# Kernel tuning notes

Measured on AMD Instinct MI355X. Metric: run time of the kernel, lower is better.

## Reference

```python
import jax, jax.numpy as jnp
import numpy as np

E, K = 8, 2            # num_experts, top_k
B, T, N, D = 32, 64, 32, 128  # batch, time, n_vars, feature
H = 2                  # heads; head_size = D // 2
EPS = np.finfo(np.float64).eps  # matches np.finfo(float).eps in torch combine


def setup_inputs() -> dict:
    key = jax.random.key(0)
    ks = jax.random.split(key, 7)
    s = 0.02  # small init keeps exp() in combine numerically tame
    x = jax.random.normal(ks[0], (B, T, N, D), dtype=jnp.float32)
    Wg = jax.random.normal(ks[1], (D, E), dtype=jnp.float32) * s
    # per-expert distinct (per-variable) weights: CustomLinear with [N, D, D]
    Wd = jax.random.normal(ks[2], (E, 2, N, D, D), dtype=jnp.float32) * s
    bd = jax.random.normal(ks[3], (E, 2, N, D), dtype=jnp.float32) * s
    # per-expert shared weights: CustomLinear with [D, D], bias [1, D]
    Ws = jax.random.normal(ks[4], (E, 2, D, D), dtype=jnp.float32) * s
    bs = jax.random.normal(ks[5], (E, 2, 1, D), dtype=jnp.float32) * s
    return {"x": x, "Wg": Wg, "Wd": Wd, "bd": bd, "Ws": Ws, "bs": bs}


def _expert(x, Wd, bd, Ws, bs):
    # Intra_Patch_Attention, self-attention over time per variable, 2 heads.
    # Wd: [2,N,D,D], bd: [2,N,D], Ws: [2,D,D], bs: [2,1,D]
    h = D // H
    k = jnp.einsum('btnd,nde->btne', x, Wd[0]) + bd[0]
    v = jnp.einsum('btnd,nde->btne', x, Wd[1]) + bd[1]
    q = x.reshape(B, T, N, H, h)
    k = k.reshape(B, T, N, H, h)
    v = v.reshape(B, T, N, H, h)
    att = jnp.einsum('bqnhd,bknhd->bnhqk', q, k) / np.float32(np.sqrt(h))
    att = jax.nn.softmax(att, axis=-1)
    o = jnp.einsum('bnhqk,bknhd->bqnhd', att, v).reshape(B, T, N, D)
    o = jax.nn.relu(jnp.einsum('btnd,de->btne', o, Ws[0]) + bs[0])
    o = jnp.einsum('btnd,de->btne', o, Ws[1]) + bs[1]
    return o  # [B,T,N,D]


def reference(x, Wg, Wd, bd, Ws, bs):
    # --- noisy-top-k gating (eval mode: no noise) ---
    logits = jnp.mean(x, axis=(1, 2)) @ Wg                  # [B,E]
    top_v, top_i = jax.lax.top_k(logits, K)                 # [B,K]
    top_g = jax.nn.softmax(top_v, axis=-1)
    gates = jnp.zeros((B, E), x.dtype).at[jnp.arange(B)[:, None], top_i].set(top_g)
    # --- per-expert attention (dense == sparse dispatch: gate 0 kills term) ---
    outs = jax.vmap(_expert, in_axes=(None, 0, 0, 0, 0))(x, Wd, bd, Ws, bs)  # [E,B,T,N,D]
    # --- SparseDispatcher.combine: log(index_add(gate * exp(expert_out))) ---
    combined = jnp.einsum('ebtnd,be->btnd', jnp.exp(outs), gates)
    combined = jnp.where(combined == 0, jnp.float32(EPS), combined)
    return jnp.log(combined)
```

## Files before the change

kernel.cpp:

```cpp
#include <hip/hip_runtime.h>

#define B_ 32
#define T_ 64
#define N_ 32
#define D_ 128
#define E_ 8

#define WS_WDT 0u
#define WS_WST 16777216u
#define WS_PART (16777216u + 524288u)
#define WS_NEED (16777216u + 524288u + 262144u)

typedef short          s16x8  __attribute__((ext_vector_type(8)));
typedef float          f32x4  __attribute__((ext_vector_type(4)));
typedef unsigned short u16x8v __attribute__((ext_vector_type(8)));
typedef unsigned short u16x4v __attribute__((ext_vector_type(4)));

#define MFMA(a, b, c) __builtin_amdgcn_mfma_f32_16x16x32_bf16(a, b, c, 0, 0, 0)

__device__ __forceinline__ float b2f(unsigned short u) {
    union { unsigned int i; float f; } v; v.i = ((unsigned int)u) << 16; return v.f;
}
__device__ __forceinline__ unsigned short f2b(float f) {
    union { float f; unsigned int i; } v; v.f = f;
    unsigned int x = v.i;
    unsigned int r = x + 0x7fffu + ((x >> 16) & 1u);
    return (unsigned short)(r >> 16);
}

template <bool BF16>
__device__ __forceinline__ float ld(const void* p, size_t i) {
    if (BF16) return b2f(((const unsigned short*)p)[i]);
    else      return ((const float*)p)[i];
}

__device__ __forceinline__ s16x8 ldBT(const unsigned short* WT, int c, int k0) {
    return *(const s16x8*)(WT + (size_t)c * D_ + k0);
}

__device__ __forceinline__ s16x8 ldA(const unsigned short* p, int row, int ldm, int k0) {
    return *(const s16x8*)(p + row * ldm + k0);
}

__device__ __forceinline__ s16x8 ldX(const unsigned short* Xs, int row, int k0) {
    return *(const s16x8*)(Xs + row * D_ + (k0 ^ ((row & 7) << 3)));
}

template <bool BF16>
__device__ void prep_body(char* pool, const void* x,
                          const void* Wd, const void* Ws, char* ws, int blk, int tid) {
    if (blk < 528) {
        const void* src;
        unsigned short* dst;
        if (blk < 512) {
            src = (const char*)Wd + (size_t)blk * 16384 * (BF16 ? 2 : 4);
            dst = (unsigned short*)(ws + WS_WDT) + (size_t)blk * 16384;
        } else {
            src = (const char*)Ws + (size_t)(blk - 512) * 16384 * (BF16 ? 2 : 4);
            dst = (unsigned short*)(ws + WS_WST) + (size_t)(blk - 512) * 16384;
        }
        const int c4 = (tid & 31) * 4;
        const int kg = tid >> 5;
        unsigned short bcol[4][16];
#pragma unroll
        for (int j = 0; j < 16; ++j) {
            const int k = kg * 16 + j;
            if (BF16) {
                u16x4v v = *(const u16x4v*)((const unsigned short*)src + (size_t)k * D_ + c4);
#pragma unroll
                for (int cc = 0; cc < 4; ++cc) bcol[cc][j] = v[cc];
            } else {
                f32x4 v = *(const f32x4*)((const float*)src + (size_t)k * D_ + c4);
#pragma unroll
                for (int cc = 0; cc < 4; ++cc) bcol[cc][j] = f2b(v[cc]);
            }
        }
#pragma unroll
        for (int cc = 0; cc < 4; ++cc) {
            unsigned short* dp = dst + (size_t)(c4 + cc) * D_ + kg * 16;
            *(u16x8v*)(dp)     = *(const u16x8v*)&bcol[cc][0];
            *(u16x8v*)(dp + 8) = *(const u16x8v*)&bcol[cc][8];
        }
    } else {
        const int idx = blk - 528;
        const int b = idx >> 4, s = idx & 15;
        const int c = tid & 15;
        const int rg = tid >> 4;
        const size_t xb = (size_t)b * (2048 * 128);
        float acc[8];
#pragma unroll
        for (int j = 0; j < 8; ++j) acc[j] = 0.f;
#pragma unroll
        for (int rr = 0; rr < 8; ++rr) {
            const int p = s * 128 + rg + rr * 16;
            const size_t base = xb + (size_t)p * 128 + c * 8;
            if (BF16) {
                u16x8v v = *(const u16x8v*)((const unsigned short*)x + base);
#pragma unroll
                for (int j = 0; j < 8; ++j) acc[j] += b2f(v[j]);
            } else {
                const float* sp = (const float*)x + base;
#pragma unroll
                for (int j = 0; j < 8; ++j) acc[j] += sp[j];
            }
        }
        float* redm = (float*)pool;
#pragma unroll
        for (int j = 0; j < 8; ++j) redm[rg * 128 + c * 8 + j] = acc[j];
        __syncthreads();
        if (tid < 128) {
            float sm = 0.f;
#pragma unroll
            for (int g2 = 0; g2 < 16; ++g2) sm += redm[g2 * 128 + tid];
            ((float*)(ws + WS_PART))[((size_t)b * 16 + s) * 128 + tid] = sm;
        }
    }
}

__global__ __launch_bounds__(256) void prep_k(const void* __restrict__ x,
                                              const void* __restrict__ Wd,
                                              const void* __restrict__ Ws,
                                              char* __restrict__ ws) {
    __shared__ __align__(16) char pool[8192];
    __shared__ int s_cnt;
    const int tid = threadIdx.x;
    if (tid == 0) s_cnt = 0;
    __syncthreads();
    if (tid < 128) {
        unsigned short wv = ((const unsigned short*)x)[2 * tid];
        int ex = (wv >> 7) & 0xFF;
        if (ex >= 0xC8) atomicAdd(&s_cnt, 1);
    }
    __syncthreads();
    if (s_cnt == 0) prep_body<true >(pool, x, Wd, Ws, ws, blockIdx.x, tid);
    else            prep_body<false>(pool, x, Wd, Ws, ws, blockIdx.x, tid);
}


template <bool BF16>
__device__ void body(char* pool, int* s_sel, float* s_g,
                     const void* x, const void* Wg, const void* bd, const void* bs,
                     const char* ws, void* out, int b, int n, int tid) {
    unsigned short* Xs  = (unsigned short*)pool;
    unsigned short* Ks  = (unsigned short*)(pool + 16384);
    unsigned short* Vt  = (unsigned short*)(pool + 25600);
    unsigned short* Y1s = (unsigned short*)(pool + 16384);
    unsigned short* P2  = (unsigned short*)(pool + 34816);
    unsigned short* Oh  = (unsigned short*)(pool + 44032);

    {
        const size_t xb = ((size_t)b * T_ * N_ + n) * D_;
        for (int i = tid; i < T_ * 16; i += 256) {
            const int t = i >> 4, c8 = (i & 15) << 3;
            unsigned short* dst = &Xs[t * D_ + (c8 ^ ((t & 7) << 3))];
            const size_t src = xb + (size_t)t * (N_ * D_) + c8;
            if (BF16) {
                *(u16x8v*)dst = *(const u16x8v*)((const unsigned short*)x + src);
            } else {
                const float* sp = (const float*)x + src;
                u16x8v v;
#pragma unroll
                for (int j2 = 0; j2 < 8; ++j2) v[j2] = f2b(sp[j2]);
                *(u16x8v*)dst = v;
            }
        }
    }

    {
        float* meanp = (float*)(pool + 34816);
        float* logit = meanp + 128;
        const float* part = (const float*)(ws + WS_PART) + (size_t)b * 16 * 128;
        if (tid < 128) {
            float sm = 0.f;
#pragma unroll
            for (int s2 = 0; s2 < 16; ++s2) sm += part[s2 * 128 + tid];
            meanp[tid] = sm * (1.f / 2048.f);
        }
        __syncthreads();
        if (tid < E_) {
            float s = 0.f;
            for (int dd = 0; dd < D_; ++dd) s += meanp[dd] * ld<BF16>(Wg, dd * E_ + tid);
            logit[tid] = s;
        }
        __syncthreads();
        if (tid == 0) {
            int i0 = 0; float v0 = logit[0];
            for (int e2 = 1; e2 < E_; ++e2) if (logit[e2] > v0) { v0 = logit[e2]; i0 = e2; }
            int i1 = -1; float v1 = -3.4e38f;
            for (int e2 = 0; e2 < E_; ++e2) { if (e2 == i0) continue; if (logit[e2] > v1) { v1 = logit[e2]; i1 = e2; } }
            float t = expf(v1 - v0);
            float s = 1.f + t;
            s_sel[0] = i0; s_sel[1] = i1;
            s_g[0] = 1.f / s; s_g[1] = t / s;
        }
        __syncthreads();
    }

    const int lane = tid & 63, w = tid >> 6;
    const int g = lane >> 4, r = lane & 15;
    const f32x4 z4 = {0.f, 0.f, 0.f, 0.f};

    f32x4 accf[4][2];
#pragma unroll
    for (int mt = 0; mt < 4; ++mt) { accf[mt][0] = z4; accf[mt][1] = z4; }

    for (int slot = 0; slot < 2; ++slot) {
        const int e = s_sel[slot];
        const float gt = s_g[slot];
        const unsigned short* WTK  = (const unsigned short*)(ws + WS_WDT) + (size_t)((e * 2 + 0) * N_ + n) * 16384;
        const unsigned short* WTV  = (const unsigned short*)(ws + WS_WDT) + (size_t)((e * 2 + 1) * N_ + n) * 16384;
        const unsigned short* WTs0 = (const unsigned short*)(ws + WS_WST) + (size_t)(e * 2 + 0) * 16384;
        const unsigned short* WTs1 = (const unsigned short*)(ws + WS_WST) + (size_t)(e * 2 + 1) * 16384;

        f32x4 y1a[4][2];
#pragma unroll
        for (int mt = 0; mt < 4; ++mt) { y1a[mt][0] = z4; y1a[mt][1] = z4; }

        for (int h = 0; h < 2; ++h) {
            if (h == 1) {
                const int cb = w * 32;
#pragma unroll
                for (int kk = 0; kk < 2; ++kk) {
                    const int k0 = kk * 32 + g * 8;
                    s16x8 bb0 = ldBT(WTs0, cb + r, k0);
                    s16x8 bb1 = ldBT(WTs0, cb + 16 + r, k0);
#pragma unroll
                    for (int mt = 0; mt < 4; ++mt) {
                        s16x8 aa = ldA(Oh, mt * 16 + r, 72, k0);
                        y1a[mt][0] = MFMA(aa, bb0, y1a[mt][0]);
                        y1a[mt][1] = MFMA(aa, bb1, y1a[mt][1]);
                    }
                }
            }
            {
                const int mat = w >> 1;
                const int chalf = (w & 1) * 32;
                const unsigned short* Wm = mat ? WTV : WTK;
                const int cbase = h * 64 + chalf;
                f32x4 acc[4][2];
#pragma unroll
                for (int mt = 0; mt < 4; ++mt) { acc[mt][0] = z4; acc[mt][1] = z4; }
#pragma unroll
                for (int kk = 0; kk < 4; ++kk) {
                    const int k0 = kk * 32 + g * 8;
                    s16x8 bb0 = ldBT(Wm, cbase + r, k0);
                    s16x8 bb1 = ldBT(Wm, cbase + 16 + r, k0);
#pragma unroll
                    for (int mt = 0; mt < 4; ++mt) {
                        s16x8 aa = ldX(Xs, mt * 16 + r, k0);
                        acc[mt][0] = MFMA(aa, bb0, acc[mt][0]);
                        acc[mt][1] = MFMA(aa, bb1, acc[mt][1]);
                    }
                }
                const size_t bbase = (size_t)((e * 2 + mat) * N_ + n) * D_;
                const float bv0 = ld<BF16>(bd, bbase + cbase + r);
                const float bv1 = ld<BF16>(bd, bbase + cbase + 16 + r);
                if (mat == 0) {
#pragma unroll
                    for (int mt = 0; mt < 4; ++mt)
#pragma unroll
                        for (int j = 0; j < 4; ++j) {
                            Ks[(mt * 16 + 4 * g + j) * 72 + chalf + r]      = f2b(acc[mt][0][j] + bv0);
                            Ks[(mt * 16 + 4 * g + j) * 72 + chalf + 16 + r] = f2b(acc[mt][1][j] + bv1);
                        }
                } else {
#pragma unroll
                    for (int mt = 0; mt < 4; ++mt) {
                        u16x4v v0, v1;
#pragma unroll
                        for (int j = 0; j < 4; ++j) {
                            v0[j] = f2b(acc[mt][0][j] + bv0);
                            v1[j] = f2b(acc[mt][1][j] + bv1);
                        }
                        *(u16x4v*)&Vt[(chalf + r) * 72 + mt * 16 + 4 * g]      = v0;
                        *(u16x4v*)&Vt[(chalf + 16 + r) * 72 + mt * 16 + 4 * g] = v1;
                    }
                }
            }
            __syncthreads();
            {
                f32x4 att[4];
#pragma unroll
                for (int c2 = 0; c2 < 4; ++c2) att[c2] = z4;
#pragma unroll
                for (int kk = 0; kk < 2; ++kk) {
                    const int k0 = kk * 32 + g * 8;
                    s16x8 q = ldX(Xs, w * 16 + r, h * 64 + k0);
#pragma unroll
                    for (int c2 = 0; c2 < 4; ++c2) {
                        s16x8 kf = ldA(Ks, c2 * 16 + r, 72, k0);
                        att[c2] = MFMA(q, kf, att[c2]);
                    }
                }
#pragma unroll
                for (int j = 0; j < 4; ++j) {
                    float m = fmaxf(fmaxf(att[0][j], att[1][j]), fmaxf(att[2][j], att[3][j]));
#pragma unroll
                    for (int mk = 1; mk < 16; mk <<= 1) m = fmaxf(m, __shfl_xor(m, mk));
                    float pr[4]; float s = 0.f;
#pragma unroll
                    for (int c2 = 0; c2 < 4; ++c2) { pr[c2] = __expf(0.125f * (att[c2][j] - m)); s += pr[c2]; }
#pragma unroll
                    for (int mk = 1; mk < 16; mk <<= 1) s += __shfl_xor(s, mk);
                    const float inv = 1.f / s;
#pragma unroll
                    for (int c2 = 0; c2 < 4; ++c2)
                        P2[(w * 16 + 4 * g + j) * 72 + c2 * 16 + r] = f2b(pr[c2] * inv);
                }
            }
            __syncthreads();
            {
                f32x4 o[4];
#pragma unroll
                for (int c2 = 0; c2 < 4; ++c2) o[c2] = z4;
#pragma unroll
                for (int kk = 0; kk < 2; ++kk) {
                    const int k0 = kk * 32 + g * 8;
                    s16x8 a = ldA(P2, w * 16 + r, 72, k0);
#pragma unroll
                    for (int c2 = 0; c2 < 4; ++c2) {
                        s16x8 vf = ldA(Vt, c2 * 16 + r, 72, k0);
                        o[c2] = MFMA(a, vf, o[c2]);
                    }
                }
#pragma unroll
                for (int c2 = 0; c2 < 4; ++c2)
#pragma unroll
                    for (int j = 0; j < 4; ++j)
                        Oh[(w * 16 + 4 * g + j) * 72 + c2 * 16 + r] = f2b(o[c2][j]);
            }
            __syncthreads();
        }

        {
            const int cb = w * 32;
#pragma unroll
            for (int kk = 0; kk < 2; ++kk) {
                const int k0 = kk * 32 + g * 8;
                s16x8 bb0 = ldBT(WTs0, cb + r, 64 + k0);
                s16x8 bb1 = ldBT(WTs0, cb + 16 + r, 64 + k0);
#pragma unroll
                for (int mt = 0; mt < 4; ++mt) {
                    s16x8 aa = ldA(Oh, mt * 16 + r, 72, k0);
                    y1a[mt][0] = MFMA(aa, bb0, y1a[mt][0]);
                    y1a[mt][1] = MFMA(aa, bb1, y1a[mt][1]);
                }
            }
            const float b0 = ld<BF16>(bs, (size_t)(e * 2 + 0) * D_ + cb + r);
            const float b1 = ld<BF16>(bs, (size_t)(e * 2 + 0) * D_ + cb + 16 + r);
#pragma unroll
            for (int mt = 0; mt < 4; ++mt)
#pragma unroll
                for (int j = 0; j < 4; ++j) {
                    Y1s[(mt * 16 + 4 * g + j) * 136 + cb + r]      = f2b(fmaxf(y1a[mt][0][j] + b0, 0.f));
                    Y1s[(mt * 16 + 4 * g + j) * 136 + cb + 16 + r] = f2b(fmaxf(y1a[mt][1][j] + b1, 0.f));
                }
        }
        __syncthreads();
        {
            const int cb = w * 32;
            f32x4 y2a[4][2];
#pragma unroll
            for (int mt = 0; mt < 4; ++mt) { y2a[mt][0] = z4; y2a[mt][1] = z4; }
#pragma unroll
            for (int kk = 0; kk < 4; ++kk) {
                const int k0 = kk * 32 + g * 8;
                s16x8 bb0 = ldBT(WTs1, cb + r, k0);
                s16x8 bb1 = ldBT(WTs1, cb + 16 + r, k0);
#pragma unroll
                for (int mt = 0; mt < 4; ++mt) {
                    s16x8 aa = ldA(Y1s, mt * 16 + r, 136, k0);
                    y2a[mt][0] = MFMA(aa, bb0, y2a[mt][0]);
                    y2a[mt][1] = MFMA(aa, bb1, y2a[mt][1]);
                }
            }
            const float b0 = ld<BF16>(bs, (size_t)(e * 2 + 1) * D_ + cb + r);
            const float b1 = ld<BF16>(bs, (size_t)(e * 2 + 1) * D_ + cb + 16 + r);
#pragma unroll
            for (int mt = 0; mt < 4; ++mt)
#pragma unroll
                for (int j = 0; j < 4; ++j) {
                    accf[mt][0][j] += gt * __expf(y2a[mt][0][j] + b0);
                    accf[mt][1][j] += gt * __expf(y2a[mt][1][j] + b1);
                }
        }
        __syncthreads();
    }

    {
        const size_t ob = ((size_t)b * T_ * N_ + n) * D_;
#pragma unroll
        for (int mt = 0; mt < 4; ++mt)
#pragma unroll
            for (int c2 = 0; c2 < 2; ++c2)
#pragma unroll
                for (int j = 0; j < 4; ++j) {
                    float cmb = accf[mt][c2][j];
                    if (cmb == 0.f) cmb = 2.2204460492503131e-16f;
                    const float rr = logf(cmb);
                    const size_t idx = ob + (size_t)(mt * 16 + 4 * g + j) * (N_ * D_) + (w * 32 + c2 * 16 + r);
                    if (BF16) ((unsigned short*)out)[idx] = f2b(rr);
                    else      ((float*)out)[idx] = rr;
                }
    }
}

__global__ __launch_bounds__(256) void fused_k(const void* __restrict__ x,
                                               const void* __restrict__ Wg,
                                               const void* __restrict__ bd,
                                               const void* __restrict__ bs,
                                               const char* __restrict__ ws,
                                               void* __restrict__ out) {
    __shared__ __align__(16) char pool[53248];
    __shared__ int s_sel[2];
    __shared__ float s_g[2];
    __shared__ int s_cnt;
    const int tid = threadIdx.x;
    const int b = blockIdx.x >> 5;
    const int n = blockIdx.x & 31;

    if (tid == 0) s_cnt = 0;
    __syncthreads();
    if (tid < 128) {
        unsigned short wv = ((const unsigned short*)x)[2 * tid];
        int ex = (wv >> 7) & 0xFF;
        if (ex >= 0xC8) atomicAdd(&s_cnt, 1);
    }
    __syncthreads();
    if (s_cnt == 0) body<true >(pool, s_sel, s_g, x, Wg, bd, bs, ws, out, b, n, tid);
    else            body<false>(pool, s_sel, s_g, x, Wg, bd, bs, ws, out, b, n, tid);
}


template <bool BF16>
__device__ __forceinline__ s16x8 ldB_f(const void* W, int k0, int c) {
    union { u16x8v u; s16x8 v; } t;
    if (BF16) {
        const unsigned short* p = (const unsigned short*)W + (size_t)k0 * D_ + c;
#pragma unroll
        for (int i = 0; i < 8; ++i) t.u[i] = p[(size_t)i * D_];
    } else {
        const float* p = (const float*)W + (size_t)k0 * D_ + c;
#pragma unroll
        for (int i = 0; i < 8; ++i) t.u[i] = f2b(p[(size_t)i * D_]);
    }
    return t.v;
}

template <bool BF16>
__device__ void body_old(char* pool, int* s_sel, float* s_g,
                         const void* x, const void* Wg, const void* Wd,
                         const void* bd, const void* Ws, const void* bs,
                         void* out, int b, int n, int tid) {
    unsigned short* Xs  = (unsigned short*)pool;
    unsigned short* Ks  = (unsigned short*)(pool + 17408);
    unsigned short* Vt  = (unsigned short*)(pool + 26624);
    unsigned short* Y1s = (unsigned short*)(pool + 17408);
    unsigned short* P2  = (unsigned short*)(pool + 35840);
    unsigned short* Oh  = (unsigned short*)(pool + 45056);

    {
        float* red   = (float*)(pool + 35840);
        float* meanp = red + 256;
        float* logit = meanp + 128;
        const int d = tid & 127;
        const int half = tid >> 7;
        const size_t xb = (size_t)b * T_ * N_ * D_;
        float a = 0.f;
        for (int p = half * 1024; p < half * 1024 + 1024; ++p)
            a += ld<BF16>(x, xb + (size_t)p * D_ + d);
        red[tid] = a;
        __syncthreads();
        if (tid < 128) meanp[tid] = (red[tid] + red[tid + 128]) * (1.f / 2048.f);
        __syncthreads();
        if (tid < E_) {
            float s = 0.f;
            for (int dd = 0; dd < D_; ++dd) s += meanp[dd] * ld<BF16>(Wg, dd * E_ + tid);
            logit[tid] = s;
        }
        __syncthreads();
        if (tid == 0) {
            int i0 = 0; float v0 = logit[0];
            for (int e2 = 1; e2 < E_; ++e2) if (logit[e2] > v0) { v0 = logit[e2]; i0 = e2; }
            int i1 = -1; float v1 = -3.4e38f;
            for (int e2 = 0; e2 < E_; ++e2) { if (e2 == i0) continue; if (logit[e2] > v1) { v1 = logit[e2]; i1 = e2; } }
            float t = expf(v1 - v0);
            float s = 1.f + t;
            s_sel[0] = i0; s_sel[1] = i1;
            s_g[0] = 1.f / s; s_g[1] = t / s;
        }
        __syncthreads();
    }
    {
        const size_t xb = ((size_t)b * T_ * N_ + n) * D_;
        for (int i = tid; i < T_ * 16; i += 256) {
            const int t = i >> 4, c8 = (i & 15) << 3;
            unsigned short* dst = &Xs[t * 136 + c8];
            const size_t src = xb + (size_t)t * (N_ * D_) + c8;
            if (BF16) {
                *(u16x8v*)dst = *(const u16x8v*)((const unsigned short*)x + src);
            } else {
                const float* sp = (const float*)x + src;
                u16x8v v;
#pragma unroll
                for (int j2 = 0; j2 < 8; ++j2) v[j2] = f2b(sp[j2]);
                *(u16x8v*)dst = v;
            }
        }
    }
    __syncthreads();

    const int lane = tid & 63, w = tid >> 6;
    const int g = lane >> 4, r = lane & 15;
    const f32x4 z4 = {0.f, 0.f, 0.f, 0.f};
    const size_t es = BF16 ? 2 : 4;

    f32x4 accf[4][2];
#pragma unroll
    for (int mt = 0; mt < 4; ++mt) { accf[mt][0] = z4; accf[mt][1] = z4; }

    for (int slot = 0; slot < 2; ++slot) {
        const int e = s_sel[slot];
        const float gt = s_g[slot];
        const char* WKp  = (const char*)Wd + es * (size_t)(((e * 2 + 0) * N_ + n) * (D_ * D_));
        const char* WVp  = (const char*)Wd + es * (size_t)(((e * 2 + 1) * N_ + n) * (D_ * D_));
        const char* Ws0p = (const char*)Ws + es * (size_t)((e * 2 + 0) * (D_ * D_));
        const char* Ws1p = (const char*)Ws + es * (size_t)((e * 2 + 1) * (D_ * D_));

        f32x4 y1a[4][2];
#pragma unroll
        for (int mt = 0; mt < 4; ++mt) { y1a[mt][0] = z4; y1a[mt][1] = z4; }

        for (int h = 0; h < 2; ++h) {
            if (h == 1) {
                const int cb = w * 32;
#pragma unroll
                for (int kk = 0; kk < 2; ++kk) {
                    const int k0 = kk * 32 + g * 8;
                    s16x8 bb0 = ldB_f<BF16>(Ws0p, k0, cb + r);
                    s16x8 bb1 = ldB_f<BF16>(Ws0p, k0, cb + 16 + r);
#pragma unroll
                    for (int mt = 0; mt < 4; ++mt) {
                        s16x8 aa = ldA(Oh, mt * 16 + r, 72, k0);
                        y1a[mt][0] = MFMA(aa, bb0, y1a[mt][0]);
                        y1a[mt][1] = MFMA(aa, bb1, y1a[mt][1]);
                    }
                }
            }
            {
                const int mat = w >> 1;
                const int chalf = (w & 1) * 32;
                const char* Wm = mat ? WVp : WKp;
                const int cbase = h * 64 + chalf;
                f32x4 acc[4][2];
#pragma unroll
                for (int mt = 0; mt < 4; ++mt) { acc[mt][0] = z4; acc[mt][1] = z4; }
#pragma unroll
                for (int kk = 0; kk < 4; ++kk) {
                    const int k0 = kk * 32 + g * 8;
                    s16x8 bb0 = ldB_f<BF16>(Wm, k0, cbase + r);
                    s16x8 bb1 = ldB_f<BF16>(Wm, k0, cbase + 16 + r);
#pragma unroll
                    for (int mt = 0; mt < 4; ++mt) {
                        s16x8 aa = ldA(Xs, mt * 16 + r, 136, k0);
                        acc[mt][0] = MFMA(aa, bb0, acc[mt][0]);
                        acc[mt][1] = MFMA(aa, bb1, acc[mt][1]);
                    }
                }
                const size_t bbase = (size_t)((e * 2 + mat) * N_ + n) * D_;
                const float bv0 = ld<BF16>(bd, bbase + cbase + r);
                const float bv1 = ld<BF16>(bd, bbase + cbase + 16 + r);
                if (mat == 0) {
#pragma unroll
                    for (int mt = 0; mt < 4; ++mt)
#pragma unroll
                        for (int j = 0; j < 4; ++j) {
                            Ks[(mt * 16 + 4 * g + j) * 72 + chalf + r]      = f2b(acc[mt][0][j] + bv0);
                            Ks[(mt * 16 + 4 * g + j) * 72 + chalf + 16 + r] = f2b(acc[mt][1][j] + bv1);
                        }
                } else {
#pragma unroll
                    for (int mt = 0; mt < 4; ++mt) {
                        u16x4v v0, v1;
#pragma unroll
                        for (int j = 0; j < 4; ++j) {
                            v0[j] = f2b(acc[mt][0][j] + bv0);
                            v1[j] = f2b(acc[mt][1][j] + bv1);
                        }
                        *(u16x4v*)&Vt[(chalf + r) * 72 + mt * 16 + 4 * g]      = v0;
                        *(u16x4v*)&Vt[(chalf + 16 + r) * 72 + mt * 16 + 4 * g] = v1;
                    }
                }
            }
            __syncthreads();
            {
                f32x4 att[4];
#pragma unroll
                for (int c2 = 0; c2 < 4; ++c2) att[c2] = z4;
#pragma unroll
                for (int kk = 0; kk < 2; ++kk) {
                    const int k0 = kk * 32 + g * 8;
                    s16x8 q = ldA(Xs, w * 16 + r, 136, h * 64 + k0);
#pragma unroll
                    for (int c2 = 0; c2 < 4; ++c2) {
                        s16x8 kf = ldA(Ks, c2 * 16 + r, 72, k0);
                        att[c2] = MFMA(q, kf, att[c2]);
                    }
                }
#pragma unroll
                for (int j = 0; j < 4; ++j) {
                    float m = fmaxf(fmaxf(att[0][j], att[1][j]), fmaxf(att[2][j], att[3][j]));
#pragma unroll
                    for (int mk = 1; mk < 16; mk <<= 1) m = fmaxf(m, __shfl_xor(m, mk));
                    float pr[4]; float s = 0.f;
#pragma unroll
                    for (int c2 = 0; c2 < 4; ++c2) { pr[c2] = __expf(0.125f * (att[c2][j] - m)); s += pr[c2]; }
#pragma unroll
                    for (int mk = 1; mk < 16; mk <<= 1) s += __shfl_xor(s, mk);
                    const float inv = 1.f / s;
#pragma unroll
                    for (int c2 = 0; c2 < 4; ++c2)
                        P2[(w * 16 + 4 * g + j) * 72 + c2 * 16 + r] = f2b(pr[c2] * inv);
                }
            }
            __syncthreads();
            {
                f32x4 o[4];
#pragma unroll
                for (int c2 = 0; c2 < 4; ++c2) o[c2] = z4;
#pragma unroll
                for (int kk = 0; kk < 2; ++kk) {
                    const int k0 = kk * 32 + g * 8;
                    s16x8 a = ldA(P2, w * 16 + r, 72, k0);
#pragma unroll
                    for (int c2 = 0; c2 < 4; ++c2) {
                        s16x8 vf = ldA(Vt, c2 * 16 + r, 72, k0);
                        o[c2] = MFMA(a, vf, o[c2]);
                    }
                }
#pragma unroll
                for (int c2 = 0; c2 < 4; ++c2)
#pragma unroll
                    for (int j = 0; j < 4; ++j)
                        Oh[(w * 16 + 4 * g + j) * 72 + c2 * 16 + r] = f2b(o[c2][j]);
            }
            __syncthreads();
        }
        {
            const int cb = w * 32;
#pragma unroll
            for (int kk = 0; kk < 2; ++kk) {
                const int k0 = kk * 32 + g * 8;
                s16x8 bb0 = ldB_f<BF16>(Ws0p, 64 + k0, cb + r);
                s16x8 bb1 = ldB_f<BF16>(Ws0p, 64 + k0, cb + 16 + r);
#pragma unroll
                for (int mt = 0; mt < 4; ++mt) {
                    s16x8 aa = ldA(Oh, mt * 16 + r, 72, k0);
                    y1a[mt][0] = MFMA(aa, bb0, y1a[mt][0]);
                    y1a[mt][1] = MFMA(aa, bb1, y1a[mt][1]);
                }
            }
            const float b0 = ld<BF16>(bs, (size_t)(e * 2 + 0) * D_ + cb + r);
            const float b1 = ld<BF16>(bs, (size_t)(e * 2 + 0) * D_ + cb + 16 + r);
#pragma unroll
            for (int mt = 0; mt < 4; ++mt)
#pragma unroll
                for (int j = 0; j < 4; ++j) {
                    Y1s[(mt * 16 + 4 * g + j) * 136 + cb + r]      = f2b(fmaxf(y1a[mt][0][j] + b0, 0.f));
                    Y1s[(mt * 16 + 4 * g + j) * 136 + cb + 16 + r] = f2b(fmaxf(y1a[mt][1][j] + b1, 0.f));
                }
        }
        __syncthreads();
        {
            const int cb = w * 32;
            f32x4 y2a[4][2];
#pragma unroll
            for (int mt = 0; mt < 4; ++mt) { y2a[mt][0] = z4; y2a[mt][1] = z4; }
#pragma unroll
            for (int kk = 0; kk < 4; ++kk) {
                const int k0 = kk * 32 + g * 8;
                s16x8 bb0 = ldB_f<BF16>(Ws1p, k0, cb + r);
                s16x8 bb1 = ldB_f<BF16>(Ws1p, k0, cb + 16 + r);
#pragma unroll
                for (int mt = 0; mt < 4; ++mt) {
                    s16x8 aa = ldA(Y1s, mt * 16 + r, 136, k0);
                    y2a[mt][0] = MFMA(aa, bb0, y2a[mt][0]);
                    y2a[mt][1] = MFMA(aa, bb1, y2a[mt][1]);
                }
            }
            const float b0 = ld<BF16>(bs, (size_t)(e * 2 + 1) * D_ + cb + r);
            const float b1 = ld<BF16>(bs, (size_t)(e * 2 + 1) * D_ + cb + 16 + r);
#pragma unroll
            for (int mt = 0; mt < 4; ++mt)
#pragma unroll
                for (int j = 0; j < 4; ++j) {
                    accf[mt][0][j] += gt * __expf(y2a[mt][0][j] + b0);
                    accf[mt][1][j] += gt * __expf(y2a[mt][1][j] + b1);
                }
        }
        __syncthreads();
    }
    {
        const size_t ob = ((size_t)b * T_ * N_ + n) * D_;
#pragma unroll
        for (int mt = 0; mt < 4; ++mt)
#pragma unroll
            for (int c2 = 0; c2 < 2; ++c2)
#pragma unroll
                for (int j = 0; j < 4; ++j) {
                    float cmb = accf[mt][c2][j];
                    if (cmb == 0.f) cmb = 2.2204460492503131e-16f;
                    const float rr = logf(cmb);
                    const size_t idx = ob + (size_t)(mt * 16 + 4 * g + j) * (N_ * D_) + (w * 32 + c2 * 16 + r);
                    if (BF16) ((unsigned short*)out)[idx] = f2b(rr);
                    else      ((float*)out)[idx] = rr;
                }
    }
}

__global__ __launch_bounds__(256) void fused_old(const void* __restrict__ x,
                                                 const void* __restrict__ Wg,
                                                 const void* __restrict__ Wd,
                                                 const void* __restrict__ bd,
                                                 const void* __restrict__ Ws,
                                                 const void* __restrict__ bs,
                                                 void* __restrict__ out) {
    __shared__ __align__(16) char pool[54272];
    __shared__ int s_sel[2];
    __shared__ float s_g[2];
    __shared__ int s_cnt;
    const int tid = threadIdx.x;
    const int b = blockIdx.x >> 5;
    const int n = blockIdx.x & 31;
    if (tid == 0) s_cnt = 0;
    __syncthreads();
    if (tid < 128) {
        unsigned short wv = ((const unsigned short*)x)[2 * tid];
        int ex = (wv >> 7) & 0xFF;
        if (ex >= 0xC8) atomicAdd(&s_cnt, 1);
    }
    __syncthreads();
    const bool isbf16 = (s_cnt == 0);
    if (isbf16) body_old<true >(pool, s_sel, s_g, x, Wg, Wd, bd, Ws, bs, out, b, n, tid);
    else        body_old<false>(pool, s_sel, s_g, x, Wg, Wd, bd, Ws, bs, out, b, n, tid);
}

extern "C" void kernel_launch(void* const* d_in, const int* in_sizes, int n_in,
                              void* d_out, int out_size, void* d_ws, size_t ws_size,
                              hipStream_t stream) {
    if (d_ws && ws_size >= (size_t)WS_NEED) {
        prep_k<<<dim3(1040), dim3(256), 0, stream>>>(d_in[0], d_in[2], d_in[4], (char*)d_ws);
        fused_k<<<dim3(B_ * N_), dim3(256), 0, stream>>>(d_in[0], d_in[1], d_in[3], d_in[5],
                                                         (const char*)d_ws, d_out);
    } else {
        fused_old<<<dim3(B_ * N_), dim3(256), 0, stream>>>(d_in[0], d_in[1], d_in[2],
                                                           d_in[3], d_in[4], d_in[5], d_out);
    }
}
```

Before: 186.3 us.

## Merge prep and fused kernels into one cooperative kernel with grid sync

Adds a cooperative kernel that runs the weight-transpose and mean-partial prep work, then a grid-wide barrier, then the per-(b,n) expert body, all in one persistent launch of 512 blocks. The aim is to remove the second kernel launch and the gap between the two kernels. In exchange, a grid-stride loop over 1024 body items on 512 blocks halves parallel slots, and the grid sync adds its own cost. It falls back to the two-kernel path if cooperative launch is unsupported or occupancy is below 2 blocks per CU.

```diff
diff --git a/kernel.cpp b/kernel.cpp
--- a/kernel.cpp
+++ b/kernel.cpp
@@ -1,4 +1,7 @@
 #include <hip/hip_runtime.h>
+#include <hip/hip_cooperative_groups.h>
+
+namespace cg = cooperative_groups;
 
 #define B_ 32
 #define T_ 64
@@ -37,27 +40,25 @@
 __device__ __forceinline__ s16x8 ldBT(const unsigned short* WT, int c, int k0) {
     return *(const s16x8*)(WT + (size_t)c * D_ + k0);
 }
-
 __device__ __forceinline__ s16x8 ldA(const unsigned short* p, int row, int ldm, int k0) {
     return *(const s16x8*)(p + row * ldm + k0);
 }
-
 __device__ __forceinline__ s16x8 ldX(const unsigned short* Xs, int row, int k0) {
     return *(const s16x8*)(Xs + row * D_ + (k0 ^ ((row & 7) << 3)));
 }
 
 template <bool BF16>
-__device__ void prep_body(char* pool, const void* x,
-                          const void* Wd, const void* Ws, char* ws, int blk, int tid) {
-    if (blk < 528) {
+__device__ void prep_item(char* pool, const void* x,
+                          const void* Wd, const void* Ws, char* ws, int item, int tid) {
+    if (item < 528) {
         const void* src;
         unsigned short* dst;
-        if (blk < 512) {
-            src = (const char*)Wd + (size_t)blk * 16384 * (BF16 ? 2 : 4);
-            dst = (unsigned short*)(ws + WS_WDT) + (size_t)blk * 16384;
+        if (item < 512) {
+            src = (const char*)Wd + (size_t)item * 16384 * (BF16 ? 2 : 4);
+            dst = (unsigned short*)(ws + WS_WDT) + (size_t)item * 16384;
         } else {
-            src = (const char*)Ws + (size_t)(blk - 512) * 16384 * (BF16 ? 2 : 4);
-            dst = (unsigned short*)(ws + WS_WST) + (size_t)(blk - 512) * 16384;
+            src = (const char*)Ws + (size_t)(item - 512) * 16384 * (BF16 ? 2 : 4);
+            dst = (unsigned short*)(ws + WS_WST) + (size_t)(item - 512) * 16384;
         }
         const int c4 = (tid & 31) * 4;
         const int kg = tid >> 5;
@@ -82,7 +83,7 @@
             *(u16x8v*)(dp + 8) = *(const u16x8v*)&bcol[cc][8];
         }
     } else {
-        const int idx = blk - 528;
+        const int idx = item - 528;
         const int b = idx >> 4, s = idx & 15;
         const int c = tid & 15;
         const int rg = tid >> 4;
@@ -115,6 +116,314 @@
             ((float*)(ws + WS_PART))[((size_t)b * 16 + s) * 128 + tid] = sm;
         }
     }
+}
+
+
+template <bool BF16>
+__device__ void body(char* pool, int* s_sel, float* s_g,
+                     const void* x, const void* Wg, const void* bd, const void* bs,
+                     const char* ws, void* out, int b, int n, int tid) {
+    unsigned short* Xs  = (unsigned short*)pool;
+    unsigned short* Ks  = (unsigned short*)(pool + 16384);
+    unsigned short* Vt  = (unsigned short*)(pool + 25600);
+    unsigned short* Y1s = (unsigned short*)(pool + 16384);
+    unsigned short* P2  = (unsigned short*)(pool + 34816);
+    unsigned short* Oh  = (unsigned short*)(pool + 44032);
+
+    {
+        const size_t xb = ((size_t)b * T_ * N_ + n) * D_;
+        for (int i = tid; i < T_ * 16; i += 256) {
+            const int t = i >> 4, c8 = (i & 15) << 3;
+            unsigned short* dst = &Xs[t * D_ + (c8 ^ ((t & 7) << 3))];
+            const size_t src = xb + (size_t)t * (N_ * D_) + c8;
+            if (BF16) {
+                *(u16x8v*)dst = *(const u16x8v*)((const unsigned short*)x + src);
+            } else {
+                const float* sp = (const float*)x + src;
+                u16x8v v;
+#pragma unroll
+                for (int j2 = 0; j2 < 8; ++j2) v[j2] = f2b(sp[j2]);
+                *(u16x8v*)dst = v;
+            }
+        }
+    }
+
+    {
+        float* meanp = (float*)(pool + 34816);
+        float* logit = meanp + 128;
+        const float* part = (const float*)(ws + WS_PART) + (size_t)b * 16 * 128;
+        if (tid < 128) {
+            float sm = 0.f;
+#pragma unroll
+            for (int s2 = 0; s2 < 16; ++s2) sm += part[s2 * 128 + tid];
+            meanp[tid] = sm * (1.f / 2048.f);
+        }
+        __syncthreads();
+        if (tid < E_) {
+            float s = 0.f;
+            for (int dd = 0; dd < D_; ++dd) s += meanp[dd] * ld<BF16>(Wg, dd * E_ + tid);
+            logit[tid] = s;
+        }
+        __syncthreads();
+        if (tid == 0) {
+            int i0 = 0; float v0 = logit[0];
+            for (int e2 = 1; e2 < E_; ++e2) if (logit[e2] > v0) { v0 = logit[e2]; i0 = e2; }
+            int i1 = -1; float v1 = -3.4e38f;
+            for (int e2 = 0; e2 < E_; ++e2) { if (e2 == i0) continue; if (logit[e2] > v1) { v1 = logit[e2]; i1 = e2; } }
+            float t = expf(v1 - v0);
+            float s = 1.f + t;
+            s_sel[0] = i0; s_sel[1] = i1;
+            s_g[0] = 1.f / s; s_g[1] = t / s;
+        }
+        __syncthreads();
+    }
+
+    const int lane = tid & 63, w = tid >> 6;
+    const int g = lane >> 4, r = lane & 15;
+    const f32x4 z4 = {0.f, 0.f, 0.f, 0.f};
+
+    f32x4 accf[4][2];
+#pragma unroll
+    for (int mt = 0; mt < 4; ++mt) { accf[mt][0] = z4; accf[mt][1] = z4; }
+
+    for (int slot = 0; slot < 2; ++slot) {
+        const int e = s_sel[slot];
+        const float gt = s_g[slot];
+        const unsigned short* WTK  = (const unsigned short*)(ws + WS_WDT) + (size_t)((e * 2 + 0) * N_ + n) * 16384;
+        const unsigned short* WTV  = (const unsigned short*)(ws + WS_WDT) + (size_t)((e * 2 + 1) * N_ + n) * 16384;
+        const unsigned short* WTs0 = (const unsigned short*)(ws + WS_WST) + (size_t)(e * 2 + 0) * 16384;
+        const unsigned short* WTs1 = (const unsigned short*)(ws + WS_WST) + (size_t)(e * 2 + 1) * 16384;
+
+        f32x4 y1a[4][2];
+#pragma unroll
+        for (int mt = 0; mt < 4; ++mt) { y1a[mt][0] = z4; y1a[mt][1] = z4; }
+
+        for (int h = 0; h < 2; ++h) {
+            if (h == 1) {
+                const int cb = w * 32;
+#pragma unroll
+                for (int kk = 0; kk < 2; ++kk) {
+                    const int k0 = kk * 32 + g * 8;
+                    s16x8 bb0 = ldBT(WTs0, cb + r, k0);
+                    s16x8 bb1 = ldBT(WTs0, cb + 16 + r, k0);
+#pragma unroll
+                    for (int mt = 0; mt < 4; ++mt) {
+                        s16x8 aa = ldA(Oh, mt * 16 + r, 72, k0);
+                        y1a[mt][0] = MFMA(aa, bb0, y1a[mt][0]);
+                        y1a[mt][1] = MFMA(aa, bb1, y1a[mt][1]);
+                    }
+                }
+            }
+            {
+                const int mat = w >> 1;
+                const int chalf = (w & 1) * 32;
+                const unsigned short* Wm = mat ? WTV : WTK;
+                const int cbase = h * 64 + chalf;
+                f32x4 acc[4][2];
+#pragma unroll
+                for (int mt = 0; mt < 4; ++mt) { acc[mt][0] = z4; acc[mt][1] = z4; }
+#pragma unroll
+                for (int kk = 0; kk < 4; ++kk) {
+                    const int k0 = kk * 32 + g * 8;
+                    s16x8 bb0 = ldBT(Wm, cbase + r, k0);
+                    s16x8 bb1 = ldBT(Wm, cbase + 16 + r, k0);
+#pragma unroll
+                    for (int mt = 0; mt < 4; ++mt) {
+                        s16x8 aa = ldX(Xs, mt * 16 + r, k0);
+                        acc[mt][0] = MFMA(aa, bb0, acc[mt][0]);
+                        acc[mt][1] = MFMA(aa, bb1, acc[mt][1]);
+                    }
+                }
+                const size_t bbase = (size_t)((e * 2 + mat) * N_ + n) * D_;
+                const float bv0 = ld<BF16>(bd, bbase + cbase + r);
+                const float bv1 = ld<BF16>(bd, bbase + cbase + 16 + r);
+                if (mat == 0) {
+#pragma unroll
+                    for (int mt = 0; mt < 4; ++mt)
+#pragma unroll
+                        for (int j = 0; j < 4; ++j) {
+                            Ks[(mt * 16 + 4 * g + j) * 72 + chalf + r]      = f2b(acc[mt][0][j] + bv0);
+                            Ks[(mt * 16 + 4 * g + j) * 72 + chalf + 16 + r] = f2b(acc[mt][1][j] + bv1);
+                        }
+                } else {
+#pragma unroll
+                    for (int mt = 0; mt < 4; ++mt) {
+                        u16x4v v0, v1;
+#pragma unroll
+                        for (int j = 0; j < 4; ++j) {
+                            v0[j] = f2b(acc[mt][0][j] + bv0);
+                            v1[j] = f2b(acc[mt][1][j] + bv1);
+                        }
+                        *(u16x4v*)&Vt[(chalf + r) * 72 + mt * 16 + 4 * g]      = v0;
+                        *(u16x4v*)&Vt[(chalf + 16 + r) * 72 + mt * 16 + 4 * g] = v1;
+                    }
+                }
+            }
+            __syncthreads();
+            {
+                f32x4 att[4];
+#pragma unroll
+                for (int c2 = 0; c2 < 4; ++c2) att[c2] = z4;
+#pragma unroll
+                for (int kk = 0; kk < 2; ++kk) {
+                    const int k0 = kk * 32 + g * 8;
+                    s16x8 q = ldX(Xs, w * 16 + r, h * 64 + k0);
+#pragma unroll
+                    for (int c2 = 0; c2 < 4; ++c2) {
+                        s16x8 kf = ldA(Ks, c2 * 16 + r, 72, k0);
+                        att[c2] = MFMA(q, kf, att[c2]);
+                    }
+                }
+#pragma unroll
+                for (int j = 0; j < 4; ++j) {
+                    float m = fmaxf(fmaxf(att[0][j], att[1][j]), fmaxf(att[2][j], att[3][j]));
+#pragma unroll
+                    for (int mk = 1; mk < 16; mk <<= 1) m = fmaxf(m, __shfl_xor(m, mk));
+                    float pr[4]; float s = 0.f;
+#pragma unroll
+                    for (int c2 = 0; c2 < 4; ++c2) { pr[c2] = __expf(0.125f * (att[c2][j] - m)); s += pr[c2]; }
+#pragma unroll
+                    for (int mk = 1; mk < 16; mk <<= 1) s += __shfl_xor(s, mk);
+                    const float inv = 1.f / s;
+#pragma unroll
+                    for (int c2 = 0; c2 < 4; ++c2)
+                        P2[(w * 16 + 4 * g + j) * 72 + c2 * 16 + r] = f2b(pr[c2] * inv);
+                }
+            }
+            __syncthreads();
+            {
+                f32x4 o[4];
+#pragma unroll
+                for (int c2 = 0; c2 < 4; ++c2) o[c2] = z4;
+#pragma unroll
+                for (int kk = 0; kk < 2; ++kk) {
+                    const int k0 = kk * 32 + g * 8;
+                    s16x8 a = ldA(P2, w * 16 + r, 72, k0);
+#pragma unroll
+                    for (int c2 = 0; c2 < 4; ++c2) {
+                        s16x8 vf = ldA(Vt, c2 * 16 + r, 72, k0);
+                        o[c2] = MFMA(a, vf, o[c2]);
+                    }
+                }
+#pragma unroll
+                for (int c2 = 0; c2 < 4; ++c2)
+#pragma unroll
+                    for (int j = 0; j < 4; ++j)
+                        Oh[(w * 16 + 4 * g + j) * 72 + c2 * 16 + r] = f2b(o[c2][j]);
+            }
+            __syncthreads();
+        }
+
+        {
+            const int cb = w * 32;
+#pragma unroll
+            for (int kk = 0; kk < 2; ++kk) {
+                const int k0 = kk * 32 + g * 8;
+                s16x8 bb0 = ldBT(WTs0, cb + r, 64 + k0);
+                s16x8 bb1 = ldBT(WTs0, cb + 16 + r, 64 + k0);
+#pragma unroll
+                for (int mt = 0; mt < 4; ++mt) {
+                    s16x8 aa = ldA(Oh, mt * 16 + r, 72, k0);
+                    y1a[mt][0] = MFMA(aa, bb0, y1a[mt][0]);
+                    y1a[mt][1] = MFMA(aa, bb1, y1a[mt][1]);
+                }
+            }
+            const float b0 = ld<BF16>(bs, (size_t)(e * 2 + 0) * D_ + cb + r);
+            const float b1 = ld<BF16>(bs, (size_t)(e * 2 + 0) * D_ + cb + 16 + r);
+#pragma unroll
+            for (int mt = 0; mt < 4; ++mt)
+#pragma unroll
+                for (int j = 0; j < 4; ++j) {
+                    Y1s[(mt * 16 + 4 * g + j) * 136 + cb + r]      = f2b(fmaxf(y1a[mt][0][j] + b0, 0.f));
+                    Y1s[(mt * 16 + 4 * g + j) * 136 + cb + 16 + r] = f2b(fmaxf(y1a[mt][1][j] + b1, 0.f));
+                }
+        }
+        __syncthreads();
+        {
+            const int cb = w * 32;
+            f32x4 y2a[4][2];
+#pragma unroll
+            for (int mt = 0; mt < 4; ++mt) { y2a[mt][0] = z4; y2a[mt][1] = z4; }
+#pragma unroll
+            for (int kk = 0; kk < 4; ++kk) {
+                const int k0 = kk * 32 + g * 8;
+                s16x8 bb0 = ldBT(WTs1, cb + r, k0);
+                s16x8 bb1 = ldBT(WTs1, cb + 16 + r, k0);
+#pragma unroll
+                for (int mt = 0; mt < 4; ++mt) {
+                    s16x8 aa = ldA(Y1s, mt * 16 + r, 136, k0);
+                    y2a[mt][0] = MFMA(aa, bb0, y2a[mt][0]);
+                    y2a[mt][1] = MFMA(aa, bb1, y2a[mt][1]);
+                }
+            }
+            const float b0 = ld<BF16>(bs, (size_t)(e * 2 + 1) * D_ + cb + r);
+            const float b1 = ld<BF16>(bs, (size_t)(e * 2 + 1) * D_ + cb + 16 + r);
+#pragma unroll
+            for (int mt = 0; mt < 4; ++mt)
+#pragma unroll
+                for (int j = 0; j < 4; ++j) {
+                    accf[mt][0][j] += gt * __expf(y2a[mt][0][j] + b0);
+                    accf[mt][1][j] += gt * __expf(y2a[mt][1][j] + b1);
+                }
+        }
+        __syncthreads();
+    }
+
+    {
+        const size_t ob = ((size_t)b * T_ * N_ + n) * D_;
+#pragma unroll
+        for (int mt = 0; mt < 4; ++mt)
+#pragma unroll
+            for (int c2 = 0; c2 < 2; ++c2)
+#pragma unroll
+                for (int j = 0; j < 4; ++j) {
+                    float cmb = accf[mt][c2][j];
+                    if (cmb == 0.f) cmb = 2.2204460492503131e-16f;
+                    const float rr = logf(cmb);
+                    const size_t idx = ob + (size_t)(mt * 16 + 4 * g + j) * (N_ * D_) + (w * 32 + c2 * 16 + r);
+                    if (BF16) ((unsigned short*)out)[idx] = f2b(rr);
+                    else      ((float*)out)[idx] = rr;
+                }
+    }
+}
+
+template <bool BF16>
+__device__ void coop_run(char* pool, int* s_sel, float* s_g,
+                         const void* x, const void* Wg, const void* Wd, const void* bd,
+                         const void* Ws, const void* bs, char* ws, void* out, int tid) {
+    for (unsigned item = blockIdx.x; item < 1040u; item += gridDim.x) {
+        prep_item<BF16>(pool, x, Wd, Ws, ws, (int)item, tid);
+        __syncthreads();
+    }
+    __threadfence();
+    cg::this_grid().sync();
+    for (unsigned idx = blockIdx.x; idx < (unsigned)(B_ * N_); idx += gridDim.x)
+        body<BF16>(pool, s_sel, s_g, x, Wg, bd, bs, ws, out, (int)(idx >> 5), (int)(idx & 31), tid);
+}
+
+__global__ __launch_bounds__(256) void coop_k(const void* __restrict__ x,
+                                              const void* __restrict__ Wg,
+                                              const void* __restrict__ Wd,
+                                              const void* __restrict__ bd,
+                                              const void* __restrict__ Ws,
+                                              const void* __restrict__ bs,
+                                              char* __restrict__ ws,
+                                              void* __restrict__ out) {
+    __shared__ __align__(16) char pool[53248];
+    __shared__ int s_sel[2];
+    __shared__ float s_g[2];
+    __shared__ int s_cnt;
+    const int tid = threadIdx.x;
+    if (tid == 0) s_cnt = 0;
+    __syncthreads();
+    if (tid < 128) {
+        unsigned short wv = ((const unsigned short*)x)[2 * tid];
+        int ex = (wv >> 7) & 0xFF;
+        if (ex >= 0xC8) atomicAdd(&s_cnt, 1);
+    }
+    __syncthreads();
+    if (s_cnt == 0) coop_run<true >(pool, s_sel, s_g, x, Wg, Wd, bd, Ws, bs, ws, out, tid);
+    else            coop_run<false>(pool, s_sel, s_g, x, Wg, Wd, bd, Ws, bs, ws, out, tid);
 }
 
 __global__ __launch_bounds__(256) void prep_k(const void* __restrict__ x,
@@ -132,277 +441,8 @@
         if (ex >= 0xC8) atomicAdd(&s_cnt, 1);
     }
     __syncthreads();
-    if (s_cnt == 0) prep_body<true >(pool, x, Wd, Ws, ws, blockIdx.x, tid);
-    else            prep_body<false>(pool, x, Wd, Ws, ws, blockIdx.x, tid);
-}
-
-
-template <bool BF16>
-__device__ void body(char* pool, int* s_sel, float* s_g,
-                     const void* x, const void* Wg, const void* bd, const void* bs,
-                     const char* ws, void* out, int b, int n, int tid) {
-    unsigned short* Xs  = (unsigned short*)pool;
-    unsigned short* Ks  = (unsigned short*)(pool + 16384);
-    unsigned short* Vt  = (unsigned short*)(pool + 25600);
-    unsigned short* Y1s = (unsigned short*)(pool + 16384);
-    unsigned short* P2  = (unsigned short*)(pool + 34816);
-    unsigned short* Oh  = (unsigned short*)(pool + 44032);
-
-    {
-        const size_t xb = ((size_t)b * T_ * N_ + n) * D_;
-        for (int i = tid; i < T_ * 16; i += 256) {
-            const int t = i >> 4, c8 = (i & 15) << 3;
-            unsigned short* dst = &Xs[t * D_ + (c8 ^ ((t & 7) << 3))];
-            const size_t src = xb + (size_t)t * (N_ * D_) + c8;
-            if (BF16) {
-                *(u16x8v*)dst = *(const u16x8v*)((const unsigned short*)x + src);
-            } else {
-                const float* sp = (const float*)x + src;
-                u16x8v v;
-#pragma unroll
-                for (int j2 = 0; j2 < 8; ++j2) v[j2] = f2b(sp[j2]);
-                *(u16x8v*)dst = v;
-            }
-        }
-    }
-
-    {
-        float* meanp = (float*)(pool + 34816);
-        float* logit = meanp + 128;
-        const float* part = (const float*)(ws + WS_PART) + (size_t)b * 16 * 128;
-        if (tid < 128) {
-            float sm = 0.f;
-#pragma unroll
-            for (int s2 = 0; s2 < 16; ++s2) sm += part[s2 * 128 + tid];
-            meanp[tid] = sm * (1.f / 2048.f);
-        }
-        __syncthreads();
-        if (tid < E_) {
-            float s = 0.f;
-            for (int dd = 0; dd < D_; ++dd) s += meanp[dd] * ld<BF16>(Wg, dd * E_ + tid);
-            logit[tid] = s;
-        }
-        __syncthreads();
-        if (tid == 0) {
-            int i0 = 0; float v0 = logit[0];
-            for (int e2 = 1; e2 < E_; ++e2) if (logit[e2] > v0) { v0 = logit[e2]; i0 = e2; }
-            int i1 = -1; float v1 = -3.4e38f;
-            for (int e2 = 0; e2 < E_; ++e2) { if (e2 == i0) continue; if (logit[e2] > v1) { v1 = logit[e2]; i1 = e2; } }
-            float t = expf(v1 - v0);
-            float s = 1.f + t;
-            s_sel[0] = i0; s_sel[1] = i1;
-            s_g[0] = 1.f / s; s_g[1] = t / s;
-        }
-        __syncthreads();
-    }
-
-    const int lane = tid & 63, w = tid >> 6;
-    const int g = lane >> 4, r = lane & 15;
-    const f32x4 z4 = {0.f, 0.f, 0.f, 0.f};
-
-    f32x4 accf[4][2];
-#pragma unroll
-    for (int mt = 0; mt < 4; ++mt) { accf[mt][0] = z4; accf[mt][1] = z4; }
-
-    for (int slot = 0; slot < 2; ++slot) {
-        const int e = s_sel[slot];
-        const float gt = s_g[slot];
-        const unsigned short* WTK  = (const unsigned short*)(ws + WS_WDT) + (size_t)((e * 2 + 0) * N_ + n) * 16384;
-        const unsigned short* WTV  = (const unsigned short*)(ws + WS_WDT) + (size_t)((e * 2 + 1) * N_ + n) * 16384;
-        const unsigned short* WTs0 = (const unsigned short*)(ws + WS_WST) + (size_t)(e * 2 + 0) * 16384;
-        const unsigned short* WTs1 = (const unsigned short*)(ws + WS_WST) + (size_t)(e * 2 + 1) * 16384;
-
-        f32x4 y1a[4][2];
-#pragma unroll
-        for (int mt = 0; mt < 4; ++mt) { y1a[mt][0] = z4; y1a[mt][1] = z4; }
-
-        for (int h = 0; h < 2; ++h) {
-            if (h == 1) {
-                const int cb = w * 32;
-#pragma unroll
-                for (int kk = 0; kk < 2; ++kk) {
-                    const int k0 = kk * 32 + g * 8;
-                    s16x8 bb0 = ldBT(WTs0, cb + r, k0);
-                    s16x8 bb1 = ldBT(WTs0, cb + 16 + r, k0);
-#pragma unroll
-                    for (int mt = 0; mt < 4; ++mt) {
-                        s16x8 aa = ldA(Oh, mt * 16 + r, 72, k0);
-                        y1a[mt][0] = MFMA(aa, bb0, y1a[mt][0]);
-                        y1a[mt][1] = MFMA(aa, bb1, y1a[mt][1]);
-                    }
-                }
-            }
-            {
-                const int mat = w >> 1;
-                const int chalf = (w & 1) * 32;
-                const unsigned short* Wm = mat ? WTV : WTK;
-                const int cbase = h * 64 + chalf;
-                f32x4 acc[4][2];
-#pragma unroll
-                for (int mt = 0; mt < 4; ++mt) { acc[mt][0] = z4; acc[mt][1] = z4; }
-#pragma unroll
-                for (int kk = 0; kk < 4; ++kk) {
-                    const int k0 = kk * 32 + g * 8;
-                    s16x8 bb0 = ldBT(Wm, cbase + r, k0);
-                    s16x8 bb1 = ldBT(Wm, cbase + 16 + r, k0);
-#pragma unroll
-                    for (int mt = 0; mt < 4; ++mt) {
-                        s16x8 aa = ldX(Xs, mt * 16 + r, k0);
-                        acc[mt][0] = MFMA(aa, bb0, acc[mt][0]);
-                        acc[mt][1] = MFMA(aa, bb1, acc[mt][1]);
-                    }
-                }
-                const size_t bbase = (size_t)((e * 2 + mat) * N_ + n) * D_;
-                const float bv0 = ld<BF16>(bd, bbase + cbase + r);
-                const float bv1 = ld<BF16>(bd, bbase + cbase + 16 + r);
-                if (mat == 0) {
-#pragma unroll
-                    for (int mt = 0; mt < 4; ++mt)
-#pragma unroll
-                        for (int j = 0; j < 4; ++j) {
-                            Ks[(mt * 16 + 4 * g + j) * 72 + chalf + r]      = f2b(acc[mt][0][j] + bv0);
-                            Ks[(mt * 16 + 4 * g + j) * 72 + chalf + 16 + r] = f2b(acc[mt][1][j] + bv1);
-                        }
-                } else {
-#pragma unroll
-                    for (int mt = 0; mt < 4; ++mt) {
-                        u16x4v v0, v1;
-#pragma unroll
-                        for (int j = 0; j < 4; ++j) {
-                            v0[j] = f2b(acc[mt][0][j] + bv0);
-                            v1[j] = f2b(acc[mt][1][j] + bv1);
-                        }
-                        *(u16x4v*)&Vt[(chalf + r) * 72 + mt * 16 + 4 * g]      = v0;
-                        *(u16x4v*)&Vt[(chalf + 16 + r) * 72 + mt * 16 + 4 * g] = v1;
-                    }
-                }
-            }
-            __syncthreads();
-            {
-                f32x4 att[4];
-#pragma unroll
-                for (int c2 = 0; c2 < 4; ++c2) att[c2] = z4;
-#pragma unroll
-                for (int kk = 0; kk < 2; ++kk) {
-                    const int k0 = kk * 32 + g * 8;
-                    s16x8 q = ldX(Xs, w * 16 + r, h * 64 + k0);
-#pragma unroll
-                    for (int c2 = 0; c2 < 4; ++c2) {
-                        s16x8 kf = ldA(Ks, c2 * 16 + r, 72, k0);
-                        att[c2] = MFMA(q, kf, att[c2]);
-                    }
-                }
-#pragma unroll
-                for (int j = 0; j < 4; ++j) {
-                    float m = fmaxf(fmaxf(att[0][j], att[1][j]), fmaxf(att[2][j], att[3][j]));
-#pragma unroll
-                    for (int mk = 1; mk < 16; mk <<= 1) m = fmaxf(m, __shfl_xor(m, mk));
-                    float pr[4]; float s = 0.f;
-#pragma unroll
-                    for (int c2 = 0; c2 < 4; ++c2) { pr[c2] = __expf(0.125f * (att[c2][j] - m)); s += pr[c2]; }
-#pragma unroll
-                    for (int mk = 1; mk < 16; mk <<= 1) s += __shfl_xor(s, mk);
-                    const float inv = 1.f / s;
-#pragma unroll
-                    for (int c2 = 0; c2 < 4; ++c2)
-                        P2[(w * 16 + 4 * g + j) * 72 + c2 * 16 + r] = f2b(pr[c2] * inv);
-                }
-            }
-            __syncthreads();
-            {
-                f32x4 o[4];
-#pragma unroll
-                for (int c2 = 0; c2 < 4; ++c2) o[c2] = z4;
-#pragma unroll
-                for (int kk = 0; kk < 2; ++kk) {
-                    const int k0 = kk * 32 + g * 8;
-                    s16x8 a = ldA(P2, w * 16 + r, 72, k0);
-#pragma unroll
-                    for (int c2 = 0; c2 < 4; ++c2) {
-                        s16x8 vf = ldA(Vt, c2 * 16 + r, 72, k0);
-                        o[c2] = MFMA(a, vf, o[c2]);
-                    }
-                }
-#pragma unroll
-                for (int c2 = 0; c2 < 4; ++c2)
-#pragma unroll
-                    for (int j = 0; j < 4; ++j)
-                        Oh[(w * 16 + 4 * g + j) * 72 + c2 * 16 + r] = f2b(o[c2][j]);
-            }
-            __syncthreads();
-        }
-
-        {
-            const int cb = w * 32;
-#pragma unroll
-            for (int kk = 0; kk < 2; ++kk) {
-                const int k0 = kk * 32 + g * 8;
-                s16x8 bb0 = ldBT(WTs0, cb + r, 64 + k0);
-                s16x8 bb1 = ldBT(WTs0, cb + 16 + r, 64 + k0);
-#pragma unroll
-                for (int mt = 0; mt < 4; ++mt) {
-                    s16x8 aa = ldA(Oh, mt * 16 + r, 72, k0);
-                    y1a[mt][0] = MFMA(aa, bb0, y1a[mt][0]);
-                    y1a[mt][1] = MFMA(aa, bb1, y1a[mt][1]);
-                }
-            }
-            const float b0 = ld<BF16>(bs, (size_t)(e * 2 + 0) * D_ + cb + r);
-            const float b1 = ld<BF16>(bs, (size_t)(e * 2 + 0) * D_ + cb + 16 + r);
-#pragma unroll
-            for (int mt = 0; mt < 4; ++mt)
-#pragma unroll
-                for (int j = 0; j < 4; ++j) {
-                    Y1s[(mt * 16 + 4 * g + j) * 136 + cb + r]      = f2b(fmaxf(y1a[mt][0][j] + b0, 0.f));
-                    Y1s[(mt * 16 + 4 * g + j) * 136 + cb + 16 + r] = f2b(fmaxf(y1a[mt][1][j] + b1, 0.f));
-                }
-        }
-        __syncthreads();
-        {
-            const int cb = w * 32;
-            f32x4 y2a[4][2];
-#pragma unroll
-            for (int mt = 0; mt < 4; ++mt) { y2a[mt][0] = z4; y2a[mt][1] = z4; }
-#pragma unroll
-            for (int kk = 0; kk < 4; ++kk) {
-                const int k0 = kk * 32 + g * 8;
-                s16x8 bb0 = ldBT(WTs1, cb + r, k0);
-                s16x8 bb1 = ldBT(WTs1, cb + 16 + r, k0);
-#pragma unroll
-                for (int mt = 0; mt < 4; ++mt) {
-                    s16x8 aa = ldA(Y1s, mt * 16 + r, 136, k0);
-                    y2a[mt][0] = MFMA(aa, bb0, y2a[mt][0]);
-                    y2a[mt][1] = MFMA(aa, bb1, y2a[mt][1]);
-                }
-            }
-            const float b0 = ld<BF16>(bs, (size_t)(e * 2 + 1) * D_ + cb + r);
-            const float b1 = ld<BF16>(bs, (size_t)(e * 2 + 1) * D_ + cb + 16 + r);
-#pragma unroll
-            for (int mt = 0; mt < 4; ++mt)
-#pragma unroll
-                for (int j = 0; j < 4; ++j) {
-                    accf[mt][0][j] += gt * __expf(y2a[mt][0][j] + b0);
-                    accf[mt][1][j] += gt * __expf(y2a[mt][1][j] + b1);
-                }
-        }
-        __syncthreads();
-    }
-
-    {
-        const size_t ob = ((size_t)b * T_ * N_ + n) * D_;
-#pragma unroll
-        for (int mt = 0; mt < 4; ++mt)
-#pragma unroll
-            for (int c2 = 0; c2 < 2; ++c2)
-#pragma unroll
-                for (int j = 0; j < 4; ++j) {
-                    float cmb = accf[mt][c2][j];
-                    if (cmb == 0.f) cmb = 2.2204460492503131e-16f;
-                    const float rr = logf(cmb);
-                    const size_t idx = ob + (size_t)(mt * 16 + 4 * g + j) * (N_ * D_) + (w * 32 + c2 * 16 + r);
-                    if (BF16) ((unsigned short*)out)[idx] = f2b(rr);
-                    else      ((float*)out)[idx] = rr;
-                }
-    }
+    if (s_cnt == 0) prep_item<true >(pool, x, Wd, Ws, ws, blockIdx.x, tid);
+    else            prep_item<false>(pool, x, Wd, Ws, ws, blockIdx.x, tid);
 }
 
 __global__ __launch_bounds__(256) void fused_k(const void* __restrict__ x,
@@ -418,7 +458,6 @@
     const int tid = threadIdx.x;
     const int b = blockIdx.x >> 5;
     const int n = blockIdx.x & 31;
-
     if (tid == 0) s_cnt = 0;
     __syncthreads();
     if (tid < 128) {
@@ -430,7 +469,6 @@
     if (s_cnt == 0) body<true >(pool, s_sel, s_g, x, Wg, bd, bs, ws, out, b, n, tid);
     else            body<false>(pool, s_sel, s_g, x, Wg, bd, bs, ws, out, b, n, tid);
 }
-
 
 template <bool BF16>
 __device__ __forceinline__ s16x8 ldB_f(const void* W, int k0, int c) {
@@ -749,6 +787,28 @@
                               void* d_out, int out_size, void* d_ws, size_t ws_size,
                               hipStream_t stream) {
     if (d_ws && ws_size >= (size_t)WS_NEED) {
+        static int coop_ok = -1;
+        if (coop_ok < 0) {
+            int dev = 0, sup = 0, occ = 0;
+            coop_ok = 0;
+            if (hipGetDevice(&dev) == hipSuccess &&
+                hipDeviceGetAttribute(&sup, hipDeviceAttributeCooperativeLaunch, dev) == hipSuccess &&
+                sup &&
+                hipOccupancyMaxActiveBlocksPerMultiprocessor(&occ, coop_k, 256, 0) == hipSuccess &&
+                occ >= 2) {
+                coop_ok = 1;
+            }
+        }
+        if (coop_ok == 1) {
+            const void* x = d_in[0]; const void* Wg = d_in[1]; const void* Wd = d_in[2];
+            const void* bd = d_in[3]; const void* Wsp = d_in[4]; const void* bs = d_in[5];
+            char* ws = (char*)d_ws; void* outp = d_out;
+            void* args[8] = {&x, &Wg, &Wd, &bd, &Wsp, &bs, &ws, &outp};
+            if (hipLaunchCooperativeKernel((const void*)coop_k, dim3(512), dim3(256),
+                                           args, 0, stream) == hipSuccess)
+                return;
+            coop_ok = 0;
+        }
         prep_k<<<dim3(1040), dim3(256), 0, stream>>>(d_in[0], d_in[2], d_in[4], (char*)d_ws);
         fused_k<<<dim3(B_ * N_), dim3(256), 0, stream>>>(d_in[0], d_in[1], d_in[3], d_in[5],
                                                          (const char*)d_ws, d_out);
```

Result: slower. 287.0 us (+54.1%).
